# Optimization experiments

Hardware: AMD Instinct MI355X
Metric: run time of the kernel (lower is better)

Reference implementation:

```python
import jax, jax.numpy as jnp
import numpy as np

EPS = 1e-5
B, F, C, H, L, S = 8192, 128, 256, 512, 4, 10


def _gelu(x):
    return jax.nn.gelu(x, approximate=False)  # torch nn.GELU default = exact erf


def _ln(x, g, b):
    m = jnp.mean(x, axis=-1, keepdims=True)
    v = jnp.var(x, axis=-1, keepdims=True)  # biased, matches torch LayerNorm
    return (x - m) / jnp.sqrt(v + EPS) * g + b


def setup_inputs() -> dict:
    key = jax.random.key(0)
    ks = iter(jax.random.split(key, 40))

    def w(shape, fan_in):
        return jax.random.normal(next(ks), shape, jnp.float32) / np.float32(np.sqrt(fan_in))

    def z0(*s):
        return jnp.zeros(s, jnp.float32)

    return dict(
        x=jax.random.normal(next(ks), (B, F), jnp.float32),
        context=jax.random.normal(next(ks), (B, C), jnp.float32),
        u=jax.random.normal(next(ks), (S, B, F), jnp.float32),
        Wi=w((F, H), F), bi=z0(H),
        Wt1=w((1, H), 1), bt1=z0(H), Wt2=w((H, H), H), bt2=z0(H),
        Wc1=w((C, 2 * H), C), bc1=z0(2 * H), Wc2=w((2 * H, H), 2 * H), bc2=z0(H),
        Wv=w((L, H, H), H), bv=z0(L, H), Woa=w((L, H, H), H), boa=z0(L, H),
        g1=jnp.ones((L, H), jnp.float32), be1=z0(L, H),
        Wm1=w((L, H, 4 * H), H), bm1=z0(L, 4 * H),
        Wm2=w((L, 4 * H, H), 4 * H), bm2=z0(L, H),
        g2=jnp.ones((L, H), jnp.float32), be2=z0(L, H),
        Wcv=w((L, H, H), H), bcv=z0(L, H), Wco=w((L, H, H), H), bco=z0(L, H),
        scale=0.5 * jnp.ones((L,), jnp.float32),
        Wp1=w((H, H), H), bp1=z0(H), Wp2=w((H, F), H), bp2=z0(F),
    )


def _forward(x, context, u, Wi, bi, Wt1, bt1, Wt2, bt2, Wc1, bc1, Wc2, bc2,
             Wv, bv, Woa, boa, g1, be1, Wm1, bm1, Wm2, bm2, g2, be2,
             Wcv, bcv, Wco, bco, scale, Wp1, bp1, Wp2, bp2):
    n_steps = u.shape[0]
    dt = 1.0 / n_steps
    nb = x.shape[0]
    nl = Wv.shape[0]

    # context projection, computed once as in torch
    ctx = _gelu(context @ Wc1 + bc1) @ Wc2 + bc2  # [B,H]
    # seq_len==1 cross-attention: softmax over a single key == 1, so the output
    # is out_proj(v_proj(ctx)) and does not depend on x -> precompute per layer.
    vctx = jnp.einsum('bh,lhk->lbk', ctx, Wcv) + bcv[:, None, :]    # [L,B,H]
    xatt = jnp.einsum('lbh,lhk->lbk', vctx, Wco) + bco[:, None, :]  # [L,B,H]

    def vel(z, t):
        tt = jnp.clip(t, 0.0, 1.0)[:, None]                          # [B,1]
        h = z @ Wi + bi + (_gelu(tt @ Wt1 + bt1) @ Wt2 + bt2)        # [B,H]
        for l in range(nl):
            # seq_len==1 self-attention collapses to out_proj(v_proj(h))
            attn = (h @ Wv[l] + bv[l]) @ Woa[l] + boa[l]
            h = _ln(h + attn, g1[l], be1[l])
            mlp = _gelu(h @ Wm1[l] + bm1[l]) @ Wm2[l] + bm2[l]
            h = _ln(h + mlp, g2[l], be2[l])
            h = h + scale[l] * xatt[l]
        return _gelu(h @ Wp1 + bp1) @ Wp2 + bp2                      # [B,F]

    def step(carry, inp):
        z, ld = carry
        t_val, u_k = inp
        t = jnp.full((nb,), t_val, jnp.float32)
        zs = jax.lax.stop_gradient(z)  # matches z.detach()/leaf z_req in torch
        v, Ju = jax.jvp(lambda zz: vel(zz, t), (zs,), (u_k,))
        ld = ld + jnp.sum(u_k * Ju, axis=-1) * dt  # Hutchinson u^T J u
        return (zs + v * dt, ld), None

    ts = jnp.arange(n_steps, dtype=jnp.float32) * dt
    (z, log_det), _ = jax.lax.scan(step, (x, jnp.zeros((nb,), jnp.float32)), (ts, u))
    return z, log_det


def reference(x, context, u, Wi, bi, Wt1, bt1, Wt2, bt2, Wc1, bc1, Wc2, bc2,
              Wv, bv, Woa, boa, g1, be1, Wm1, bm1, Wm2, bm2, g2, be2,
              Wcv, bcv, Wco, bco, scale, Wp1, bp1, Wp2, bp2):
    return _forward(x, context, u, Wi, bi, Wt1, bt1, Wt2, bt2, Wc1, bc1, Wc2, bc2,
                    Wv, bv, Woa, boa, g1, be1, Wm1, bm1, Wm2, bm2, g2, be2,
                    Wcv, bcv, Wco, bco, scale, Wp1, bp1, Wp2, bp2)
```

## Files before the change

kernel.cpp:

```cpp
#include <hip/hip_runtime.h>
#include <math.h>

using floatx4 = __attribute__((ext_vector_type(4))) float;
using bf16x8  = __attribute__((ext_vector_type(8))) __bf16;
using ushort8 = __attribute__((ext_vector_type(8))) unsigned short;

__device__ __forceinline__ float b2f(unsigned short u) {
  unsigned v = ((unsigned)u) << 16; float f; __builtin_memcpy(&f, &v, 4); return f;
}
__device__ __forceinline__ unsigned short f2b(float f) {
  unsigned u; __builtin_memcpy(&u, &f, 4);
  u += 0x7fffu + ((u >> 16) & 1u);
  return (unsigned short)(u >> 16);
}
__device__ __forceinline__ float gelu_f(float x) {
  return 0.5f * x * (1.0f + erff(x * 0.7071067811865475f));
}
__device__ __forceinline__ float gelu_d(float x) {
  float cdf = 0.5f * (1.0f + erff(x * 0.7071067811865475f));
  float pdf = 0.3989422804014327f * expf(-0.5f * x * x);
  return cdf + x * pdf;
}
__device__ __forceinline__ void gload16(const unsigned short* g, unsigned short* l) {
  __builtin_amdgcn_global_load_lds(
      (__attribute__((address_space(1))) void*)(g),
      (__attribute__((address_space(3))) void*)(l), 16, 0, 0);
}

template<int MODE>
__global__ __launch_bounds__(256) void gemm_bt_k(
    const unsigned short* __restrict__ A, const unsigned short* __restrict__ Bt,
    void* __restrict__ C, const float* __restrict__ bias,
    const float* __restrict__ bias2, int M, int N, int K)
{
  __shared__ unsigned short As[128 * 32];
  __shared__ unsigned short Bs[128 * 32];
  const int tid  = threadIdx.x;
  const int lane = tid & 63;
  const int wave = tid >> 6;
  const int row0 = blockIdx.y * 128;
  const int col0 = blockIdx.x * 128;

  const int sr = wave * 32 + (lane >> 2);
  const int sk = (lane & 3) * 8;
  const unsigned short* Ag0 = A  + (size_t)(row0 + sr) * K + sk;
  const unsigned short* Ag1 = Ag0 + (size_t)16 * K;
  const unsigned short* Bg0 = Bt + (size_t)(col0 + sr) * K + sk;
  const unsigned short* Bg1 = Bg0 + (size_t)16 * K;
  unsigned short* As0 = &As[wave * 1024];
  unsigned short* Bs0 = &Bs[wave * 1024];

  const int wr = wave >> 1, wc = wave & 1;
  const int mrow = lane & 15;
  const int kq = (lane >> 4) * 8;

  floatx4 acc[4][4];
  const floatx4 zf4 = {0.f, 0.f, 0.f, 0.f};
  #pragma unroll
  for (int i = 0; i < 4; i++)
    #pragma unroll
    for (int j = 0; j < 4; j++) acc[i][j] = zf4;

  for (int k0 = 0; k0 < K; k0 += 32) {
    __syncthreads();
    gload16(Ag0 + k0, As0);
    gload16(Ag1 + k0, As0 + 512);
    gload16(Bg0 + k0, Bs0);
    gload16(Bg1 + k0, Bs0 + 512);
    __syncthreads();
    bf16x8 af[4], bfr[4];
    #pragma unroll
    for (int t = 0; t < 4; t++)
      af[t] = *(const bf16x8*)&As[(wr * 64 + t * 16 + mrow) * 32 + kq];
    #pragma unroll
    for (int t = 0; t < 4; t++)
      bfr[t] = *(const bf16x8*)&Bs[(wc * 64 + t * 16 + mrow) * 32 + kq];
    #pragma unroll
    for (int i = 0; i < 4; i++)
      #pragma unroll
      for (int j = 0; j < 4; j++)
        acc[i][j] = __builtin_amdgcn_mfma_f32_16x16x32_bf16(af[i], bfr[j], acc[i][j], 0, 0, 0);
  }

  const int quad = lane >> 4;
  const int cl = lane & 15;
  #pragma unroll
  for (int j = 0; j < 4; j++) {
    int col = col0 + wc * 64 + j * 16 + cl;
    float bb = bias ? bias[col] : 0.f;
    if (MODE >= 2) { if (bias2) bb += bias2[col]; }
    #pragma unroll
    for (int i = 0; i < 4; i++) {
      int rbase = row0 + wr * 64 + i * 16 + quad * 4;
      if (MODE == 3) {
        #pragma unroll
        for (int pp = 0; pp < 2; pp++) {
          float p = acc[i][j][2 * pp] + bb;
          float t = acc[i][j][2 * pp + 1];
          ((unsigned short*)C)[(size_t)(rbase + 2 * pp) * N + col]     = f2b(gelu_f(p));
          ((unsigned short*)C)[(size_t)(rbase + 2 * pp + 1) * N + col] = f2b(gelu_d(p) * t);
        }
      } else {
        #pragma unroll
        for (int rr = 0; rr < 4; rr++) {
          int row = rbase + rr;
          float v = acc[i][j][rr];
          if (MODE == 0 || MODE == 1) v += bb;
          if (MODE == 2) { if ((row & 1) == 0) v += bb; }
          if (MODE == 1) v = gelu_f(v);
          ((unsigned short*)C)[(size_t)row * N + col] = f2b(v);
        }
      }
    }
  }
}

template<bool XATT>
__global__ __launch_bounds__(256) void gemm_ln_k(
    const unsigned short* __restrict__ A, const unsigned short* __restrict__ Bt,
    unsigned short* __restrict__ h, const float* __restrict__ bias,
    const float* __restrict__ g, const float* __restrict__ be,
    const unsigned short* __restrict__ xatt, const float* __restrict__ sc_p,
    int K)
{
  constexpr int N = 512;
  __shared__ unsigned short As[32 * 32];
  __shared__ unsigned short Bs[512 * 32];
  __shared__ unsigned short Hs[32 * 512];
  __shared__ float red[16][4][4];
  const int tid = threadIdx.x, lane = tid & 63, wave = tid >> 6;
  const int row0 = blockIdx.x * 32;

  #pragma unroll
  for (int t = 0; t < 8; t++) {
    int r = wave * 8 + t;
    gload16(h + (size_t)(row0 + r) * N + lane * 8, &Hs[r * N]);
  }

  const int srb = lane >> 2;
  const int sk  = (lane & 3) * 8;
  const int mrow = lane & 15, kq = (lane >> 4) * 8;

  floatx4 acc[2][8];
  const floatx4 zf4 = {0.f, 0.f, 0.f, 0.f};
  #pragma unroll
  for (int i = 0; i < 2; i++)
    #pragma unroll
    for (int j = 0; j < 8; j++) acc[i][j] = zf4;

  for (int k0 = 0; k0 < K; k0 += 32) {
    __syncthreads();
    if (wave < 2)
      gload16(A + (size_t)(row0 + wave * 16 + srb) * K + k0 + sk, &As[wave * 512]);
    #pragma unroll
    for (int t = 0; t < 8; t++) {
      int n = wave * 128 + t * 16;
      gload16(Bt + (size_t)(n + srb) * K + k0 + sk, &Bs[n * 32]);
    }
    __syncthreads();
    bf16x8 af[2], bfr[8];
    #pragma unroll
    for (int i = 0; i < 2; i++)
      af[i] = *(const bf16x8*)&As[(i * 16 + mrow) * 32 + kq];
    #pragma unroll
    for (int j = 0; j < 8; j++)
      bfr[j] = *(const bf16x8*)&Bs[(wave * 128 + j * 16 + mrow) * 32 + kq];
    #pragma unroll
    for (int i = 0; i < 2; i++)
      #pragma unroll
      for (int j = 0; j < 8; j++)
        acc[i][j] = __builtin_amdgcn_mfma_f32_16x16x32_bf16(af[i], bfr[j], acc[i][j], 0, 0, 0);
  }

  const int quad = lane >> 4, cl = lane & 15;
  float bc[8], gc[8], bec[8];
  #pragma unroll
  for (int j = 0; j < 8; j++) {
    int col = wave * 128 + j * 16 + cl;
    bc[j] = bias[col]; gc[j] = g[col]; bec[j] = be[col];
  }

  #pragma unroll
  for (int i = 0; i < 2; i++) {
    #pragma unroll
    for (int rp = 0; rp < 2; rp++) {
      int re = i * 16 + quad * 4 + rp * 2;
      float sx = 0.f, sxx = 0.f, sdv = 0.f, sxdv = 0.f;
      #pragma unroll
      for (int j = 0; j < 8; j++) {
        int col = wave * 128 + j * 16 + cl;
        float xp = acc[i][j][rp * 2]     + bc[j] + b2f(Hs[re * N + col]);
        float dv = acc[i][j][rp * 2 + 1]         + b2f(Hs[(re + 1) * N + col]);
        sx += xp; sxx += xp * xp; sdv += dv; sxdv += xp * dv;
      }
      #pragma unroll
      for (int off = 1; off <= 8; off <<= 1) {
        sx   += __shfl_xor(sx, off, 64);
        sxx  += __shfl_xor(sxx, off, 64);
        sdv  += __shfl_xor(sdv, off, 64);
        sxdv += __shfl_xor(sxdv, off, 64);
      }
      if (cl == 0) {
        int pr = i * 8 + quad * 2 + rp;
        red[pr][wave][0] = sx; red[pr][wave][1] = sxx;
        red[pr][wave][2] = sdv; red[pr][wave][3] = sxdv;
      }
    }
  }
  __syncthreads();

  const float inv = 1.0f / 512.0f;
  float sl = 0.f;
  if (XATT) sl = *sc_p;
  #pragma unroll
  for (int i = 0; i < 2; i++) {
    #pragma unroll
    for (int rp = 0; rp < 2; rp++) {
      int pr = i * 8 + quad * 2 + rp;
      float sx   = red[pr][0][0] + red[pr][1][0] + red[pr][2][0] + red[pr][3][0];
      float sxx  = red[pr][0][1] + red[pr][1][1] + red[pr][2][1] + red[pr][3][1];
      float sdv  = red[pr][0][2] + red[pr][1][2] + red[pr][2][2] + red[pr][3][2];
      float sxdv = red[pr][0][3] + red[pr][1][3] + red[pr][2][3] + red[pr][3][3];
      float m = sx * inv;
      float var = sxx * inv - m * m;
      float rstd = rsqrtf(var + 1e-5f);
      float dm = sdv * inv;
      float cm = (sxdv - m * sdv) * inv * rstd;
      int re = i * 16 + quad * 4 + rp * 2;
      size_t growe = (size_t)(row0 + re);
      #pragma unroll
      for (int j = 0; j < 8; j++) {
        int col = wave * 128 + j * 16 + cl;
        float xp = acc[i][j][rp * 2]     + bc[j] + b2f(Hs[re * N + col]);
        float dv = acc[i][j][rp * 2 + 1]         + b2f(Hs[(re + 1) * N + col]);
        float xh = (xp - m) * rstd;
        float y = xh * gc[j] + bec[j];
        if (XATT) y += sl * b2f(xatt[(growe >> 1) * N + col]);
        float dy = gc[j] * rstd * (dv - dm - xh * cm);
        h[growe * N + col]       = f2b(y);
        h[(growe + 1) * N + col] = f2b(dy);
      }
    }
  }
}

__global__ __launch_bounds__(256) void gemm_vout_k(
    const unsigned short* __restrict__ A, const unsigned short* __restrict__ Bt,
    const float* __restrict__ bias, const float* __restrict__ u_cur,
    const float* __restrict__ u_next, float* __restrict__ zf,
    float* __restrict__ ldb, unsigned short* __restrict__ Abuf,
    int K, float dtv)
{
  constexpr int N = 128;
  __shared__ unsigned short As[128 * 32];
  __shared__ unsigned short Bs[128 * 32];
  __shared__ float red[64][2];
  const int tid = threadIdx.x, lane = tid & 63, wave = tid >> 6;
  const int row0 = blockIdx.x * 128;

  const int sr = wave * 32 + (lane >> 2);
  const int sk = (lane & 3) * 8;
  const unsigned short* Ag0 = A  + (size_t)(row0 + sr) * K + sk;
  const unsigned short* Ag1 = Ag0 + (size_t)16 * K;
  const unsigned short* Bg0 = Bt + (size_t)sr * K + sk;
  const unsigned short* Bg1 = Bg0 + (size_t)16 * K;
  unsigned short* As0 = &As[wave * 1024];
  unsigned short* Bs0 = &Bs[wave * 1024];

  const int wr = wave >> 1, wc = wave & 1;
  const int mrow = lane & 15, kq = (lane >> 4) * 8;

  floatx4 acc[4][4];
  const floatx4 zf4 = {0.f, 0.f, 0.f, 0.f};
  #pragma unroll
  for (int i = 0; i < 4; i++)
    #pragma unroll
    for (int j = 0; j < 4; j++) acc[i][j] = zf4;

  for (int k0 = 0; k0 < K; k0 += 32) {
    __syncthreads();
    gload16(Ag0 + k0, As0);
    gload16(Ag1 + k0, As0 + 512);
    gload16(Bg0 + k0, Bs0);
    gload16(Bg1 + k0, Bs0 + 512);
    __syncthreads();
    bf16x8 af[4], bfr[4];
    #pragma unroll
    for (int t = 0; t < 4; t++)
      af[t] = *(const bf16x8*)&As[(wr * 64 + t * 16 + mrow) * 32 + kq];
    #pragma unroll
    for (int t = 0; t < 4; t++)
      bfr[t] = *(const bf16x8*)&Bs[(wc * 64 + t * 16 + mrow) * 32 + kq];
    #pragma unroll
    for (int i = 0; i < 4; i++)
      #pragma unroll
      for (int j = 0; j < 4; j++)
        acc[i][j] = __builtin_amdgcn_mfma_f32_16x16x32_bf16(af[i], bfr[j], acc[i][j], 0, 0, 0);
  }

  const int quad = lane >> 4, cl = lane & 15;
  #pragma unroll
  for (int i = 0; i < 4; i++) {
    #pragma unroll
    for (int rp = 0; rp < 2; rp++) {
      int rloc_e = wr * 64 + i * 16 + quad * 4 + rp * 2;
      size_t growe = (size_t)(row0 + rloc_e);
      size_t b = growe >> 1;
      float dacc = 0.f;
      #pragma unroll
      for (int j = 0; j < 4; j++) {
        int col = wc * 64 + j * 16 + cl;
        float v  = acc[i][j][rp * 2] + bias[col];
        float Ju = acc[i][j][rp * 2 + 1];
        float z = zf[b * N + col] + v * dtv;
        zf[b * N + col] = z;
        Abuf[growe * N + col] = f2b(z);
        if (u_next) Abuf[(growe + 1) * N + col] = f2b(u_next[b * N + col]);
        dacc += u_cur[b * N + col] * Ju;
      }
      #pragma unroll
      for (int off = 1; off <= 8; off <<= 1) dacc += __shfl_xor(dacc, off, 64);
      if (cl == 0) red[wr * 32 + i * 8 + quad * 2 + rp][wc] = dacc;
    }
  }
  __syncthreads();
  if (tid < 64) ldb[(row0 >> 1) + tid] += (red[tid][0] + red[tid][1]) * dtv;
}

__global__ void transpose_cast_k(const float* __restrict__ W,
                                 unsigned short* __restrict__ Wt, int K, int N)
{
  __shared__ float tile[32][33];
  size_t off = (size_t)blockIdx.z * K * N;
  const float* Wp = W + off;
  unsigned short* Wtp = Wt + off;
  int bx = blockIdx.x, by = blockIdx.y;
  int tx = threadIdx.x, ty = threadIdx.y;
  #pragma unroll
  for (int i = ty; i < 32; i += 8)
    tile[i][tx] = Wp[(size_t)(by * 32 + i) * N + bx * 32 + tx];
  __syncthreads();
  #pragma unroll
  for (int i = ty; i < 32; i += 8)
    Wtp[(size_t)(bx * 32 + i) * K + by * 32 + tx] = f2b(tile[tx][i]);
}

__global__ __launch_bounds__(256) void combine_bias_k(
    const float* __restrict__ bvp, const float* __restrict__ Wb,
    const float* __restrict__ bo, float* __restrict__ bout, int H)
{
  int out = blockIdx.x * blockDim.x + threadIdx.x;
  int l   = blockIdx.y;
  const float* A2 = Wb + (size_t)l * H * H;
  float s = bo[(size_t)l * H + out];
  for (int k = 0; k < H; k++) s += bvp[(size_t)l * H + k] * A2[(size_t)k * H + out];
  bout[(size_t)l * H + out] = s;
}

__global__ __launch_bounds__(256) void cast_k(const float* __restrict__ in,
                                              unsigned short* __restrict__ out, size_t n) {
  size_t i = blockIdx.x * blockDim.x + threadIdx.x;
  if (i < n) out[i] = f2b(in[i]);
}

__global__ __launch_bounds__(512) void temb_all_k(
    const float* __restrict__ Wt1, const float* __restrict__ bt1,
    const float* __restrict__ Wt2, const float* __restrict__ bt2,
    float dtv, float* __restrict__ tvecs, int H)
{
  __shared__ float e[512];
  int j = threadIdx.x;
  float t = fminf(fmaxf((float)blockIdx.x * dtv, 0.f), 1.f);
  e[j] = gelu_f(t * Wt1[j] + bt1[j]);
  __syncthreads();
  float s = bt2[j];
  for (int k = 0; k < H; k++) s += e[k] * Wt2[(size_t)k * H + j];
  tvecs[(size_t)blockIdx.x * H + j] = s;
}

__global__ __launch_bounds__(256) void init_k(
    const float* __restrict__ x, const float* __restrict__ u0,
    float* __restrict__ zf, float* __restrict__ ld,
    unsigned short* __restrict__ Abuf, int BF, int Bsz, int F)
{
  int i = (int)(blockIdx.x * blockDim.x + threadIdx.x);
  if (i < BF) {
    int r = i / F, c = i - r * F;
    float v = x[i];
    zf[i] = v;
    Abuf[(size_t)(2 * r) * F + c]     = f2b(v);
    Abuf[(size_t)(2 * r + 1) * F + c] = f2b(u0[i]);
  }
  if (i < Bsz) ld[i] = 0.f;
}

__global__ __launch_bounds__(256) void final_k(
    const float* __restrict__ zf, const float* __restrict__ ld,
    float* __restrict__ out, int BF, int Bsz)
{
  int i = (int)(blockIdx.x * blockDim.x + threadIdx.x);
  if (i < BF) out[i] = zf[i];
  if (i < Bsz) out[BF + i] = ld[i];
}

extern "C" void kernel_launch(void* const* d_in, const int* in_sizes, int n_in,
                              void* d_out, int out_size, void* d_ws, size_t ws_size,
                              hipStream_t stream) {
  constexpr int B = 8192, F = 128, C = 256, H = 512, L = 4, S = 10;
  constexpr int B2 = 2 * B;
  constexpr int BF = B * F;
  const float dtv = 1.0f / S;

  const float* x    = (const float*)d_in[0];
  const float* ctxI = (const float*)d_in[1];
  const float* u    = (const float*)d_in[2];
  const float* Wi   = (const float*)d_in[3];
  const float* bi   = (const float*)d_in[4];
  const float* Wt1  = (const float*)d_in[5];
  const float* bt1  = (const float*)d_in[6];
  const float* Wt2  = (const float*)d_in[7];
  const float* bt2  = (const float*)d_in[8];
  const float* Wc1  = (const float*)d_in[9];
  const float* bc1  = (const float*)d_in[10];
  const float* Wc2  = (const float*)d_in[11];
  const float* bc2  = (const float*)d_in[12];
  const float* Wv   = (const float*)d_in[13];
  const float* bv   = (const float*)d_in[14];
  const float* Woa  = (const float*)d_in[15];
  const float* boa  = (const float*)d_in[16];
  const float* g1   = (const float*)d_in[17];
  const float* be1  = (const float*)d_in[18];
  const float* Wm1  = (const float*)d_in[19];
  const float* bm1  = (const float*)d_in[20];
  const float* Wm2  = (const float*)d_in[21];
  const float* bm2  = (const float*)d_in[22];
  const float* g2   = (const float*)d_in[23];
  const float* be2  = (const float*)d_in[24];
  const float* Wcv  = (const float*)d_in[25];
  const float* bcv  = (const float*)d_in[26];
  const float* Wco  = (const float*)d_in[27];
  const float* bco  = (const float*)d_in[28];
  const float* scal = (const float*)d_in[29];
  const float* Wp1  = (const float*)d_in[30];
  const float* bp1  = (const float*)d_in[31];
  const float* Wp2  = (const float*)d_in[32];
  const float* bp2  = (const float*)d_in[33];

  char* wp = (char*)d_ws;
  auto alloc = [&](size_t bytes) -> void* {
    void* r = (void*)wp;
    wp += (bytes + 255) & ~(size_t)255;
    return r;
  };
  unsigned short* wWit  = (unsigned short*)alloc((size_t)H * F * 2);
  unsigned short* wWc1t = (unsigned short*)alloc((size_t)2 * H * C * 2);
  unsigned short* wWc2t = (unsigned short*)alloc((size_t)H * 2 * H * 2);
  unsigned short* wWvoT = (unsigned short*)alloc((size_t)L * H * H * 2);
  unsigned short* wCtxT = (unsigned short*)alloc((size_t)L * H * H * 2);
  unsigned short* wWm1t = (unsigned short*)alloc((size_t)L * 4 * H * H * 2);
  unsigned short* wWm2t = (unsigned short*)alloc((size_t)L * H * 4 * H * 2);
  unsigned short* wWp1t = (unsigned short*)alloc((size_t)H * H * 2);
  unsigned short* wWp2t = (unsigned short*)alloc((size_t)F * H * 2);
  unsigned short* wOaT  = (unsigned short*)alloc((size_t)L * H * H * 2);
  unsigned short* wCoT  = (unsigned short*)alloc((size_t)L * H * H * 2);
  unsigned short* wVb   = (unsigned short*)alloc((size_t)L * H * H * 2);
  unsigned short* wCvb  = (unsigned short*)alloc((size_t)L * H * H * 2);
  float* bvo            = (float*)alloc((size_t)L * H * 4);
  float* cbvo           = (float*)alloc((size_t)L * H * 4);
  float* tvecs          = (float*)alloc((size_t)S * H * 4);
  unsigned short* ctxc  = (unsigned short*)alloc((size_t)B * C * 2);
  unsigned short* Abuf  = (unsigned short*)alloc((size_t)B2 * F * 2);
  unsigned short* hbuf  = (unsigned short*)alloc((size_t)B2 * H * 2);
  unsigned short* tmp2  = (unsigned short*)alloc((size_t)B2 * H * 2);
  unsigned short* mbuf  = (unsigned short*)alloc((size_t)B2 * 4 * H * 2);
  unsigned short* xattb = (unsigned short*)alloc((size_t)L * B * H * 2);
  float* zf             = (float*)alloc((size_t)B * F * 4);
  float* ldb            = (float*)alloc((size_t)B * 4);
  (void)ws_size; (void)in_sizes; (void)n_in; (void)out_size;

  auto T = [&](const float* W, unsigned short* Wt, int K, int N, int Lz) {
    dim3 g(N / 32, K / 32, Lz);
    transpose_cast_k<<<g, dim3(32, 8), 0, stream>>>(W, Wt, K, N);
  };
  auto G = [&](int mode, const unsigned short* A, const unsigned short* Bt, void* Cc,
               const float* bias, const float* bias2, int M, int N, int K) {
    dim3 g(N / 128, M / 128);
    switch (mode) {
      case 0: gemm_bt_k<0><<<g, 256, 0, stream>>>(A, Bt, Cc, bias, bias2, M, N, K); break;
      case 1: gemm_bt_k<1><<<g, 256, 0, stream>>>(A, Bt, Cc, bias, bias2, M, N, K); break;
      case 2: gemm_bt_k<2><<<g, 256, 0, stream>>>(A, Bt, Cc, bias, bias2, M, N, K); break;
      case 3: gemm_bt_k<3><<<g, 256, 0, stream>>>(A, Bt, Cc, bias, bias2, M, N, K); break;
    }
  };

  T(Wi,  wWit,  F, H, 1);
  T(Wc1, wWc1t, C, 2 * H, 1);
  T(Wc2, wWc2t, 2 * H, H, 1);
  T(Wm1, wWm1t, H, 4 * H, L);
  T(Wm2, wWm2t, 4 * H, H, L);
  T(Wp1, wWp1t, H, H, 1);
  T(Wp2, wWp2t, H, F, 1);
  T(Woa, wOaT, H, H, L);
  T(Wco, wCoT, H, H, L);
  cast_k<<<((size_t)L * H * H + 255) / 256, 256, 0, stream>>>(Wv,  wVb,  (size_t)L * H * H);
  cast_k<<<((size_t)L * H * H + 255) / 256, 256, 0, stream>>>(Wcv, wCvb, (size_t)L * H * H);
  for (int l = 0; l < L; l++) {
    size_t o2 = (size_t)l * H * H;
    G(0, wOaT + o2, wVb  + o2, wWvoT + o2, nullptr, nullptr, H, H, H);
    G(0, wCoT + o2, wCvb + o2, wCtxT + o2, nullptr, nullptr, H, H, H);
  }
  combine_bias_k<<<dim3(H / 256, L), 256, 0, stream>>>(bv,  Woa, boa, bvo,  H);
  combine_bias_k<<<dim3(H / 256, L), 256, 0, stream>>>(bcv, Wco, bco, cbvo, H);

  cast_k<<<(B * C + 255) / 256, 256, 0, stream>>>(ctxI, ctxc, (size_t)B * C);
  G(1, ctxc, wWc1t, mbuf, bc1, nullptr, B, 2 * H, C);
  G(0, mbuf, wWc2t, tmp2, bc2, nullptr, B, H, 2 * H);
  for (int l = 0; l < L; l++)
    G(0, tmp2, wCtxT + (size_t)l * H * H, xattb + (size_t)l * B * H,
      cbvo + l * H, nullptr, B, H, H);

  temb_all_k<<<S, H, 0, stream>>>(Wt1, bt1, Wt2, bt2, dtv, tvecs, H);
  init_k<<<(BF + 255) / 256, 256, 0, stream>>>(x, u, zf, ldb, Abuf, BF, B, F);

  for (int s = 0; s < S; s++) {
    G(2, Abuf, wWit, hbuf, bi, tvecs + (size_t)s * H, B2, H, F);
    for (int l = 0; l < L; l++) {
      size_t o2 = (size_t)l * H * H;
      size_t om = (size_t)l * 4 * H * H;
      gemm_ln_k<false><<<B2 / 32, 256, 0, stream>>>(
          hbuf, wWvoT + o2, hbuf, bvo + l * H, g1 + l * H, be1 + l * H,
          nullptr, nullptr, H);
      G(3, hbuf, wWm1t + om, mbuf, bm1 + (size_t)l * 4 * H, nullptr, B2, 4 * H, H);
      gemm_ln_k<true><<<B2 / 32, 256, 0, stream>>>(
          mbuf, wWm2t + om, hbuf, bm2 + l * H, g2 + l * H, be2 + l * H,
          xattb + (size_t)l * B * H, scal + l, 4 * H);
    }
    G(3, hbuf, wWp1t, tmp2, bp1, nullptr, B2, H, H);
    const float* u_cur = u + (size_t)s * BF;
    const float* u_next = (s + 1 < S) ? u + (size_t)(s + 1) * BF : nullptr;
    gemm_vout_k<<<B2 / 128, 256, 0, stream>>>(
        tmp2, wWp2t, bp2, u_cur, u_next, zf, ldb, Abuf, H, dtv);
  }

  final_k<<<(BF + 255) / 256, 256, 0, stream>>>(zf, ldb, (float*)d_out, BF, B);
}
```

Baseline: 9.553 ms.

## Switch GEMM kernels to 32x32x16 MFMA tiles and add XCD-aware block remap

All three GEMM kernels (generic, fused LayerNorm, velocity output) now use the 32x32x16 bf16 MFMA instruction instead of 16x16x32. The goal is fewer MFMA issues and fewer LDS fragment reads per K step. The epilogues are rewritten for the 32x32 accumulator layout, and the row-reduction shuffles widen to 32 lanes. The generic GEMM also remaps block indices so that row tiles sharing operands land on the same XCD, to improve L2 reuse. The new register layout and the interleaved primal/tangent row pairing must still line up, or the results will be wrong.

```diff
diff --git a/kernel.cpp b/kernel.cpp
--- a/kernel.cpp
+++ b/kernel.cpp
@@ -1,9 +1,10 @@
 #include <hip/hip_runtime.h>
 #include <math.h>
 
-using floatx4 = __attribute__((ext_vector_type(4))) float;
-using bf16x8  = __attribute__((ext_vector_type(8))) __bf16;
-using ushort8 = __attribute__((ext_vector_type(8))) unsigned short;
+using floatx4  = __attribute__((ext_vector_type(4))) float;
+using floatx16 = __attribute__((ext_vector_type(16))) float;
+using bf16x8   = __attribute__((ext_vector_type(8))) __bf16;
+using ushort8  = __attribute__((ext_vector_type(8))) unsigned short;
 
 __device__ __forceinline__ float b2f(unsigned short u) {
   unsigned v = ((unsigned)u) << 16; float f; __builtin_memcpy(&f, &v, 4); return f;
@@ -25,6 +26,12 @@
   __builtin_amdgcn_global_load_lds(
       (__attribute__((address_space(1))) void*)(g),
       (__attribute__((address_space(3))) void*)(l), 16, 0, 0);
+}
+__device__ __forceinline__ floatx16 zero16() {
+  floatx16 z;
+  #pragma unroll
+  for (int e = 0; e < 16; e++) z[e] = 0.f;
+  return z;
 }
 
 template<int MODE>
@@ -38,8 +45,17 @@
   const int tid  = threadIdx.x;
   const int lane = tid & 63;
   const int wave = tid >> 6;
-  const int row0 = blockIdx.y * 128;
-  const int col0 = blockIdx.x * 128;
+
+  int bx = blockIdx.x, by = blockIdx.y;
+  if ((gridDim.y & 7) == 0) {
+    int lin = by * gridDim.x + bx;
+    int xcd = lin & 7;
+    int w   = lin >> 3;
+    by = xcd * (gridDim.y >> 3) + w / gridDim.x;
+    bx = w % gridDim.x;
+  }
+  const int row0 = by * 128;
+  const int col0 = bx * 128;
 
   const int sr = wave * 32 + (lane >> 2);
   const int sk = (lane & 3) * 8;
@@ -51,15 +67,12 @@
   unsigned short* Bs0 = &Bs[wave * 1024];
 
   const int wr = wave >> 1, wc = wave & 1;
-  const int mrow = lane & 15;
-  const int kq = (lane >> 4) * 8;
-
-  floatx4 acc[4][4];
-  const floatx4 zf4 = {0.f, 0.f, 0.f, 0.f};
-  #pragma unroll
-  for (int i = 0; i < 4; i++)
-    #pragma unroll
-    for (int j = 0; j < 4; j++) acc[i][j] = zf4;
+  const int m32 = lane & 31;
+  const int kh  = (lane >> 5) * 8;
+
+  floatx16 acc[2][2];
+  acc[0][0] = zero16(); acc[0][1] = zero16();
+  acc[1][0] = zero16(); acc[1][1] = zero16();
 
   for (int k0 = 0; k0 < K; k0 += 32) {
     __syncthreads();
@@ -68,45 +81,51 @@
     gload16(Bg0 + k0, Bs0);
     gload16(Bg1 + k0, Bs0 + 512);
     __syncthreads();
-    bf16x8 af[4], bfr[4];
-    #pragma unroll
-    for (int t = 0; t < 4; t++)
-      af[t] = *(const bf16x8*)&As[(wr * 64 + t * 16 + mrow) * 32 + kq];
-    #pragma unroll
-    for (int t = 0; t < 4; t++)
-      bfr[t] = *(const bf16x8*)&Bs[(wc * 64 + t * 16 + mrow) * 32 + kq];
-    #pragma unroll
-    for (int i = 0; i < 4; i++)
-      #pragma unroll
-      for (int j = 0; j < 4; j++)
-        acc[i][j] = __builtin_amdgcn_mfma_f32_16x16x32_bf16(af[i], bfr[j], acc[i][j], 0, 0, 0);
-  }
-
-  const int quad = lane >> 4;
-  const int cl = lane & 15;
-  #pragma unroll
-  for (int j = 0; j < 4; j++) {
-    int col = col0 + wc * 64 + j * 16 + cl;
+    bf16x8 af[2][2], bfr[2][2];
+    #pragma unroll
+    for (int i = 0; i < 2; i++)
+      #pragma unroll
+      for (int h = 0; h < 2; h++)
+        af[i][h] = *(const bf16x8*)&As[(wr * 64 + i * 32 + m32) * 32 + h * 16 + kh];
+    #pragma unroll
+    for (int j = 0; j < 2; j++)
+      #pragma unroll
+      for (int h = 0; h < 2; h++)
+        bfr[j][h] = *(const bf16x8*)&Bs[(wc * 64 + j * 32 + m32) * 32 + h * 16 + kh];
+    #pragma unroll
+    for (int h = 0; h < 2; h++)
+      #pragma unroll
+      for (int i = 0; i < 2; i++)
+        #pragma unroll
+        for (int j = 0; j < 2; j++)
+          acc[i][j] = __builtin_amdgcn_mfma_f32_32x32x16_bf16(af[i][h], bfr[j][h], acc[i][j], 0, 0, 0);
+  }
+
+  const int hi = lane >> 5;
+  #pragma unroll
+  for (int j = 0; j < 2; j++) {
+    int col = col0 + wc * 64 + j * 32 + m32;
     float bb = bias ? bias[col] : 0.f;
     if (MODE >= 2) { if (bias2) bb += bias2[col]; }
     #pragma unroll
-    for (int i = 0; i < 4; i++) {
-      int rbase = row0 + wr * 64 + i * 16 + quad * 4;
+    for (int i = 0; i < 2; i++) {
+      int rb = row0 + wr * 64 + i * 32 + 4 * hi;
       if (MODE == 3) {
         #pragma unroll
-        for (int pp = 0; pp < 2; pp++) {
-          float p = acc[i][j][2 * pp] + bb;
-          float t = acc[i][j][2 * pp + 1];
-          ((unsigned short*)C)[(size_t)(rbase + 2 * pp) * N + col]     = f2b(gelu_f(p));
-          ((unsigned short*)C)[(size_t)(rbase + 2 * pp + 1) * N + col] = f2b(gelu_d(p) * t);
+        for (int pr = 0; pr < 8; pr++) {
+          int re = rb + 2 * (pr & 1) + 8 * (pr >> 1);
+          float p = acc[i][j][2 * pr] + bb;
+          float t = acc[i][j][2 * pr + 1];
+          ((unsigned short*)C)[(size_t)re * N + col]       = f2b(gelu_f(p));
+          ((unsigned short*)C)[(size_t)(re + 1) * N + col] = f2b(gelu_d(p) * t);
         }
       } else {
         #pragma unroll
-        for (int rr = 0; rr < 4; rr++) {
-          int row = rbase + rr;
-          float v = acc[i][j][rr];
+        for (int reg = 0; reg < 16; reg++) {
+          int row = rb + (reg & 3) + 8 * (reg >> 2);
+          float v = acc[i][j][reg];
           if (MODE == 0 || MODE == 1) v += bb;
-          if (MODE == 2) { if ((row & 1) == 0) v += bb; }
+          if (MODE == 2) { if ((reg & 1) == 0) v += bb; }
           if (MODE == 1) v = gelu_f(v);
           ((unsigned short*)C)[(size_t)row * N + col] = f2b(v);
         }
@@ -139,14 +158,12 @@
 
   const int srb = lane >> 2;
   const int sk  = (lane & 3) * 8;
-  const int mrow = lane & 15, kq = (lane >> 4) * 8;
-
-  floatx4 acc[2][8];
-  const floatx4 zf4 = {0.f, 0.f, 0.f, 0.f};
-  #pragma unroll
-  for (int i = 0; i < 2; i++)
-    #pragma unroll
-    for (int j = 0; j < 8; j++) acc[i][j] = zf4;
+  const int m32 = lane & 31;
+  const int kh  = (lane >> 5) * 8;
+
+  floatx16 acc[4];
+  #pragma unroll
+  for (int j = 0; j < 4; j++) acc[j] = zero16();
 
   for (int k0 = 0; k0 < K; k0 += 32) {
     __syncthreads();
@@ -158,53 +175,52 @@
       gload16(Bt + (size_t)(n + srb) * K + k0 + sk, &Bs[n * 32]);
     }
     __syncthreads();
-    bf16x8 af[2], bfr[8];
-    #pragma unroll
-    for (int i = 0; i < 2; i++)
-      af[i] = *(const bf16x8*)&As[(i * 16 + mrow) * 32 + kq];
-    #pragma unroll
-    for (int j = 0; j < 8; j++)
-      bfr[j] = *(const bf16x8*)&Bs[(wave * 128 + j * 16 + mrow) * 32 + kq];
-    #pragma unroll
-    for (int i = 0; i < 2; i++)
-      #pragma unroll
-      for (int j = 0; j < 8; j++)
-        acc[i][j] = __builtin_amdgcn_mfma_f32_16x16x32_bf16(af[i], bfr[j], acc[i][j], 0, 0, 0);
-  }
-
-  const int quad = lane >> 4, cl = lane & 15;
-  float bc[8], gc[8], bec[8];
-  #pragma unroll
-  for (int j = 0; j < 8; j++) {
-    int col = wave * 128 + j * 16 + cl;
+    bf16x8 af[2], bfr[4][2];
+    #pragma unroll
+    for (int hh = 0; hh < 2; hh++)
+      af[hh] = *(const bf16x8*)&As[m32 * 32 + hh * 16 + kh];
+    #pragma unroll
+    for (int j = 0; j < 4; j++)
+      #pragma unroll
+      for (int hh = 0; hh < 2; hh++)
+        bfr[j][hh] = *(const bf16x8*)&Bs[(wave * 128 + j * 32 + m32) * 32 + hh * 16 + kh];
+    #pragma unroll
+    for (int hh = 0; hh < 2; hh++)
+      #pragma unroll
+      for (int j = 0; j < 4; j++)
+        acc[j] = __builtin_amdgcn_mfma_f32_32x32x16_bf16(af[hh], bfr[j][hh], acc[j], 0, 0, 0);
+  }
+
+  const int hi = lane >> 5;
+  float bc[4], gc[4], bec[4];
+  #pragma unroll
+  for (int j = 0; j < 4; j++) {
+    int col = wave * 128 + j * 32 + m32;
     bc[j] = bias[col]; gc[j] = g[col]; bec[j] = be[col];
   }
 
   #pragma unroll
-  for (int i = 0; i < 2; i++) {
-    #pragma unroll
-    for (int rp = 0; rp < 2; rp++) {
-      int re = i * 16 + quad * 4 + rp * 2;
-      float sx = 0.f, sxx = 0.f, sdv = 0.f, sxdv = 0.f;
-      #pragma unroll
-      for (int j = 0; j < 8; j++) {
-        int col = wave * 128 + j * 16 + cl;
-        float xp = acc[i][j][rp * 2]     + bc[j] + b2f(Hs[re * N + col]);
-        float dv = acc[i][j][rp * 2 + 1]         + b2f(Hs[(re + 1) * N + col]);
-        sx += xp; sxx += xp * xp; sdv += dv; sxdv += xp * dv;
-      }
-      #pragma unroll
-      for (int off = 1; off <= 8; off <<= 1) {
-        sx   += __shfl_xor(sx, off, 64);
-        sxx  += __shfl_xor(sxx, off, 64);
-        sdv  += __shfl_xor(sdv, off, 64);
-        sxdv += __shfl_xor(sxdv, off, 64);
-      }
-      if (cl == 0) {
-        int pr = i * 8 + quad * 2 + rp;
-        red[pr][wave][0] = sx; red[pr][wave][1] = sxx;
-        red[pr][wave][2] = sdv; red[pr][wave][3] = sxdv;
-      }
+  for (int pr = 0; pr < 8; pr++) {
+    int re = 2 * (pr & 1) + 8 * (pr >> 1) + 4 * hi;
+    float sx = 0.f, sxx = 0.f, sdv = 0.f, sxdv = 0.f;
+    #pragma unroll
+    for (int j = 0; j < 4; j++) {
+      int col = wave * 128 + j * 32 + m32;
+      float xp = acc[j][2 * pr]     + bc[j] + b2f(Hs[re * N + col]);
+      float dv = acc[j][2 * pr + 1]         + b2f(Hs[(re + 1) * N + col]);
+      sx += xp; sxx += xp * xp; sdv += dv; sxdv += xp * dv;
+    }
+    #pragma unroll
+    for (int off = 1; off <= 16; off <<= 1) {
+      sx   += __shfl_xor(sx, off, 64);
+      sxx  += __shfl_xor(sxx, off, 64);
+      sdv  += __shfl_xor(sdv, off, 64);
+      sxdv += __shfl_xor(sxdv, off, 64);
+    }
+    if (m32 == 0) {
+      int pid = re >> 1;
+      red[pid][wave][0] = sx; red[pid][wave][1] = sxx;
+      red[pid][wave][2] = sdv; red[pid][wave][3] = sxdv;
     }
   }
   __syncthreads();
@@ -213,33 +229,30 @@
   float sl = 0.f;
   if (XATT) sl = *sc_p;
   #pragma unroll
-  for (int i = 0; i < 2; i++) {
-    #pragma unroll
-    for (int rp = 0; rp < 2; rp++) {
-      int pr = i * 8 + quad * 2 + rp;
-      float sx   = red[pr][0][0] + red[pr][1][0] + red[pr][2][0] + red[pr][3][0];
-      float sxx  = red[pr][0][1] + red[pr][1][1] + red[pr][2][1] + red[pr][3][1];
-      float sdv  = red[pr][0][2] + red[pr][1][2] + red[pr][2][2] + red[pr][3][2];
-      float sxdv = red[pr][0][3] + red[pr][1][3] + red[pr][2][3] + red[pr][3][3];
-      float m = sx * inv;
-      float var = sxx * inv - m * m;
-      float rstd = rsqrtf(var + 1e-5f);
-      float dm = sdv * inv;
-      float cm = (sxdv - m * sdv) * inv * rstd;
-      int re = i * 16 + quad * 4 + rp * 2;
-      size_t growe = (size_t)(row0 + re);
-      #pragma unroll
-      for (int j = 0; j < 8; j++) {
-        int col = wave * 128 + j * 16 + cl;
-        float xp = acc[i][j][rp * 2]     + bc[j] + b2f(Hs[re * N + col]);
-        float dv = acc[i][j][rp * 2 + 1]         + b2f(Hs[(re + 1) * N + col]);
-        float xh = (xp - m) * rstd;
-        float y = xh * gc[j] + bec[j];
-        if (XATT) y += sl * b2f(xatt[(growe >> 1) * N + col]);
-        float dy = gc[j] * rstd * (dv - dm - xh * cm);
-        h[growe * N + col]       = f2b(y);
-        h[(growe + 1) * N + col] = f2b(dy);
-      }
+  for (int pr = 0; pr < 8; pr++) {
+    int re = 2 * (pr & 1) + 8 * (pr >> 1) + 4 * hi;
+    int pid = re >> 1;
+    float sx   = red[pid][0][0] + red[pid][1][0] + red[pid][2][0] + red[pid][3][0];
+    float sxx  = red[pid][0][1] + red[pid][1][1] + red[pid][2][1] + red[pid][3][1];
+    float sdv  = red[pid][0][2] + red[pid][1][2] + red[pid][2][2] + red[pid][3][2];
+    float sxdv = red[pid][0][3] + red[pid][1][3] + red[pid][2][3] + red[pid][3][3];
+    float m = sx * inv;
+    float var = sxx * inv - m * m;
+    float rstd = rsqrtf(var + 1e-5f);
+    float dm = sdv * inv;
+    float cm = (sxdv - m * sdv) * inv * rstd;
+    size_t growe = (size_t)(row0 + re);
+    #pragma unroll
+    for (int j = 0; j < 4; j++) {
+      int col = wave * 128 + j * 32 + m32;
+      float xp = acc[j][2 * pr]     + bc[j] + b2f(Hs[re * N + col]);
+      float dv = acc[j][2 * pr + 1]         + b2f(Hs[(re + 1) * N + col]);
+      float xh = (xp - m) * rstd;
+      float y = xh * gc[j] + bec[j];
+      if (XATT) y += sl * b2f(xatt[(growe >> 1) * N + col]);
+      float dy = gc[j] * rstd * (dv - dm - xh * cm);
+      h[growe * N + col]       = f2b(y);
+      h[(growe + 1) * N + col] = f2b(dy);
     }
   }
 }
@@ -268,14 +281,12 @@
   unsigned short* Bs0 = &Bs[wave * 1024];
 
   const int wr = wave >> 1, wc = wave & 1;
-  const int mrow = lane & 15, kq = (lane >> 4) * 8;
-
-  floatx4 acc[4][4];
-  const floatx4 zf4 = {0.f, 0.f, 0.f, 0.f};
-  #pragma unroll
-  for (int i = 0; i < 4; i++)
-    #pragma unroll
-    for (int j = 0; j < 4; j++) acc[i][j] = zf4;
+  const int m32 = lane & 31;
+  const int kh  = (lane >> 5) * 8;
+
+  floatx16 acc[2][2];
+  acc[0][0] = zero16(); acc[0][1] = zero16();
+  acc[1][0] = zero16(); acc[1][1] = zero16();
 
   for (int k0 = 0; k0 < K; k0 += 32) {
     __syncthreads();
@@ -284,34 +295,40 @@
     gload16(Bg0 + k0, Bs0);
     gload16(Bg1 + k0, Bs0 + 512);
     __syncthreads();
-    bf16x8 af[4], bfr[4];
-    #pragma unroll
-    for (int t = 0; t < 4; t++)
-      af[t] = *(const bf16x8*)&As[(wr * 64 + t * 16 + mrow) * 32 + kq];
-    #pragma unroll
-    for (int t = 0; t < 4; t++)
-      bfr[t] = *(const bf16x8*)&Bs[(wc * 64 + t * 16 + mrow) * 32 + kq];
-    #pragma unroll
-    for (int i = 0; i < 4; i++)
-      #pragma unroll
-      for (int j = 0; j < 4; j++)
-        acc[i][j] = __builtin_amdgcn_mfma_f32_16x16x32_bf16(af[i], bfr[j], acc[i][j], 0, 0, 0);
-  }
-
-  const int quad = lane >> 4, cl = lane & 15;
-  #pragma unroll
-  for (int i = 0; i < 4; i++) {
-    #pragma unroll
-    for (int rp = 0; rp < 2; rp++) {
-      int rloc_e = wr * 64 + i * 16 + quad * 4 + rp * 2;
-      size_t growe = (size_t)(row0 + rloc_e);
+    bf16x8 af[2][2], bfr[2][2];
+    #pragma unroll
+    for (int i = 0; i < 2; i++)
+      #pragma unroll
+      for (int h = 0; h < 2; h++)
+        af[i][h] = *(const bf16x8*)&As[(wr * 64 + i * 32 + m32) * 32 + h * 16 + kh];
+    #pragma unroll
+    for (int j = 0; j < 2; j++)
+      #pragma unroll
+      for (int h = 0; h < 2; h++)
+        bfr[j][h] = *(const bf16x8*)&Bs[(wc * 64 + j * 32 + m32) * 32 + h * 16 + kh];
+    #pragma unroll
+    for (int h = 0; h < 2; h++)
+      #pragma unroll
+      for (int i = 0; i < 2; i++)
+        #pragma unroll
+        for (int j = 0; j < 2; j++)
+          acc[i][j] = __builtin_amdgcn_mfma_f32_32x32x16_bf16(af[i][h], bfr[j][h], acc[i][j], 0, 0, 0);
+  }
+
+  const int hi = lane >> 5;
+  #pragma unroll
+  for (int i = 0; i < 2; i++) {
+    #pragma unroll
+    for (int pr = 0; pr < 8; pr++) {
+      int re_loc = wr * 64 + i * 32 + 4 * hi + 2 * (pr & 1) + 8 * (pr >> 1);
+      size_t growe = (size_t)(row0 + re_loc);
       size_t b = growe >> 1;
       float dacc = 0.f;
       #pragma unroll
-      for (int j = 0; j < 4; j++) {
-        int col = wc * 64 + j * 16 + cl;
-        float v  = acc[i][j][rp * 2] + bias[col];
-        float Ju = acc[i][j][rp * 2 + 1];
+      for (int j = 0; j < 2; j++) {
+        int col = wc * 64 + j * 32 + m32;
+        float v  = acc[i][j][2 * pr] + bias[col];
+        float Ju = acc[i][j][2 * pr + 1];
         float z = zf[b * N + col] + v * dtv;
         zf[b * N + col] = z;
         Abuf[growe * N + col] = f2b(z);
@@ -319,8 +336,8 @@
         dacc += u_cur[b * N + col] * Ju;
       }
       #pragma unroll
-      for (int off = 1; off <= 8; off <<= 1) dacc += __shfl_xor(dacc, off, 64);
-      if (cl == 0) red[wr * 32 + i * 8 + quad * 2 + rp][wc] = dacc;
+      for (int off = 1; off <= 16; off <<= 1) dacc += __shfl_xor(dacc, off, 64);
+      if (m32 == 0) red[re_loc >> 1][wc] = dacc;
     }
   }
   __syncthreads();
```

Result: slower. 10.17 ms (+6.5%).
